# Kernel optimization log

Measured on AMD Instinct MI355X. Metric: run time of the kernel, lower is better.

The kernel has to match this reference:

```python
import jax, jax.numpy as jnp
import numpy as np

HIDDEN = 3584
N_HEADS = 28
N_KV = 4
HEAD_DIM = 128
MROPE = [16, 24, 24]          # sums to HEAD_DIM // 2
W_BITS = 4                    # per-output-channel symmetric weight fake-quant
A_BITS = 8                    # per-tensor symmetric activation fake-quant
ROPE_THETA = 1000000.0
B, S = 1, 2048


def fake_quant(x, bits, axis=None):
    """Symmetric uniform fake-quant with straight-through estimator."""
    qmax = 2.0 ** (bits - 1) - 1
    if axis is None:
        s = jnp.max(jnp.abs(x)) / qmax
    else:
        s = jnp.max(jnp.abs(x), axis=axis, keepdims=True) / qmax
    s = jnp.maximum(s, 1e-8)
    dq = jnp.clip(jnp.round(x / s), -qmax - 1.0, qmax) * s
    return x + jax.lax.stop_gradient(dq - x)


def quant_linear(x, w, b):
    """QuantLinear: fake-quant activations (per-tensor) and weights (per out-channel)."""
    xq = fake_quant(x, A_BITS)
    wq = fake_quant(w, W_BITS, axis=1)        # w: [out, in]
    y = xq @ wq.T
    return y + b if b is not None else y


def rotate_half(x):
    x1, x2 = jnp.split(x, 2, axis=-1)
    return jnp.concatenate([-x2, x1], axis=-1)


def apply_multimodal_rope(q, k, cos, sin):
    """cos/sin: (3, b, s, head_dim). Interleave t/h/w sections per mrope_section."""
    splits = np.cumsum([m * 2 for m in MROPE])[:-1]

    def mix(t):
        parts = jnp.split(t, splits, axis=-1)
        return jnp.concatenate([parts[i][i % 3] for i in range(len(parts))], axis=-1)[:, None]  # (b,1,s,hd)

    c, s_ = mix(cos), mix(sin)
    q_emb = q * c + rotate_half(q) * s_
    k_emb = k * c + rotate_half(k) * s_
    return q_emb, k_emb


def setup_inputs() -> dict:
    key = jax.random.key(0)
    ks = jax.random.split(key, 8)
    hidden_states = jax.random.normal(ks[0], (B, S, HIDDEN), dtype=jnp.float32)
    # realistic rotary embeddings, broadcast over the 3 mrope axes (text: all equal)
    inv_freq = 1.0 / (ROPE_THETA ** (np.arange(0, HEAD_DIM, 2, dtype=np.float32) / HEAD_DIM))
    pos = np.arange(S, dtype=np.float32)
    freqs = pos[:, None] * inv_freq[None, :]                  # (S, hd/2)
    emb = np.concatenate([freqs, freqs], axis=-1)             # (S, hd)
    cos = jnp.asarray(np.broadcast_to(np.cos(emb)[None, None], (3, B, S, HEAD_DIM)).copy())
    sin = jnp.asarray(np.broadcast_to(np.sin(emb)[None, None], (3, B, S, HEAD_DIM)).copy())
    sc = 0.02
    wq = jax.random.normal(ks[1], (HIDDEN, HIDDEN), dtype=jnp.float32) * sc
    bq = jax.random.normal(ks[2], (HIDDEN,), dtype=jnp.float32) * sc
    wk = jax.random.normal(ks[3], (N_KV * HEAD_DIM, HIDDEN), dtype=jnp.float32) * sc
    bk = jax.random.normal(ks[4], (N_KV * HEAD_DIM,), dtype=jnp.float32) * sc
    wv = jax.random.normal(ks[5], (N_KV * HEAD_DIM, HIDDEN), dtype=jnp.float32) * sc
    bv = jax.random.normal(ks[6], (N_KV * HEAD_DIM,), dtype=jnp.float32) * sc
    wo = jax.random.normal(ks[7], (HIDDEN, HIDDEN), dtype=jnp.float32) * sc
    return {"hidden_states": hidden_states, "cos": cos, "sin": sin,
            "wq": wq, "bq": bq, "wk": wk, "bk": bk, "wv": wv, "bv": bv, "wo": wo}


def reference(hidden_states, cos, sin, wq, bq, wk, bk, wv, bv, wo):
    b, s, _ = hidden_states.shape
    q = quant_linear(hidden_states, wq, bq).reshape(b, s, N_HEADS, HEAD_DIM).transpose(0, 2, 1, 3)
    k = quant_linear(hidden_states, wk, bk).reshape(b, s, N_KV, HEAD_DIM).transpose(0, 2, 1, 3)
    v = quant_linear(hidden_states, wv, bv).reshape(b, s, N_KV, HEAD_DIM).transpose(0, 2, 1, 3)
    q, k = apply_multimodal_rope(q, k, cos, sin)
    g = N_HEADS // N_KV
    k = jnp.repeat(k, g, axis=1)   # repeat_kv
    v = jnp.repeat(v, g, axis=1)
    scores = jnp.einsum('bhqd,bhkd->bhqk', q, k) / np.float32(np.sqrt(HEAD_DIM))
    causal = jnp.tril(jnp.ones((s, s), dtype=bool))
    scores = jnp.where(causal[None, None], scores, jnp.finfo(scores.dtype).min)
    p = jax.nn.softmax(scores, axis=-1)
    attn = jnp.einsum('bhqk,bhkd->bhqd', p, v)
    attn = attn.transpose(0, 2, 1, 3).reshape(b, s, N_HEADS * HEAD_DIM)
    return quant_linear(attn, wo, None)
```

## Files before the change

### kernel.cpp

```cpp
#include <hip/hip_runtime.h>
#include <stdint.h>


#define S_LEN 2048
#define HID   3584
#define NH    28
#define NKV   4
#define HD    128
#define GQA   7
#define KD    3584

typedef signed char i8;
typedef unsigned short u16;
typedef __attribute__((ext_vector_type(4))) int      v4i;
typedef __attribute__((ext_vector_type(4))) float    v4f;
typedef __attribute__((ext_vector_type(8))) _Float16 f16x8;
typedef __attribute__((ext_vector_type(4))) float    f32x4;

#define QK_SCALE   4096.0f
#define S_UNSCALE  5.9604644775390625e-8f
#define V_SCALE    64.0f
#define P_SCALE    16384.0f
#define O_UNSCALE  9.5367431640625e-7f

#define GLOAD_LDS(g, l) __builtin_amdgcn_global_load_lds( \
    (__attribute__((address_space(1))) void*)(g),          \
    (__attribute__((address_space(3))) void*)(l), 16, 0, 0)

static __device__ __forceinline__ u16 f16bits(_Float16 h) {
  u16 u; __builtin_memcpy(&u, &h, 2); return u;
}
static __device__ __forceinline__ void splitf16(float x, u16& hb, u16& lb) {
  _Float16 h = (_Float16)x;
  float r = x - (float)h;
  _Float16 l = (_Float16)r;
  hb = f16bits(h); lb = f16bits(l);
}

__global__ void k_zero(float* p) {
  if (threadIdx.x < 8) p[threadIdx.x] = 0.0f;
}

__global__ void k_absmax(const float* __restrict__ x, long long n, unsigned* __restrict__ out) {
  long long i0 = ((long long)blockIdx.x * blockDim.x + threadIdx.x) * 4;
  long long stride = (long long)gridDim.x * blockDim.x * 4;
  float m = 0.0f;
  for (long long i = i0; i < n; i += stride) {
    f32x4 v = *(const f32x4*)(x + i);
    m = fmaxf(m, fmaxf(fmaxf(fabsf(v.x), fabsf(v.y)), fmaxf(fabsf(v.z), fabsf(v.w))));
  }
  #pragma unroll
  for (int o = 32; o > 0; o >>= 1) m = fmaxf(m, __shfl_xor(m, o, 64));
  __shared__ float sm[4];
  if ((threadIdx.x & 63) == 0) sm[threadIdx.x >> 6] = m;
  __syncthreads();
  if (threadIdx.x == 0) {
    m = fmaxf(fmaxf(sm[0], sm[1]), fmaxf(sm[2], sm[3]));
    atomicMax(out, __float_as_uint(m));
  }
}

__global__ void k_quant_act(const float* __restrict__ x, i8* __restrict__ q,
                            const unsigned* __restrict__ amax, long long n) {
  float s = fmaxf(__uint_as_float(*amax) / 127.0f, 1e-8f);
  long long i = ((long long)blockIdx.x * blockDim.x + threadIdx.x) * 4;
  if (i >= n) return;
  f32x4 v = *(const f32x4*)(x + i);
  char4 c;
  c.x = (char)fminf(fmaxf(rintf(v.x / s), -128.0f), 127.0f);
  c.y = (char)fminf(fmaxf(rintf(v.y / s), -128.0f), 127.0f);
  c.z = (char)fminf(fmaxf(rintf(v.z / s), -128.0f), 127.0f);
  c.w = (char)fminf(fmaxf(rintf(v.w / s), -128.0f), 127.0f);
  *(char4*)(q + i) = c;
}

__global__ void k_quant_w(const float* __restrict__ w, i8* __restrict__ wq,
                          float* __restrict__ sw) {
  const int row = blockIdx.x;
  const float2* wr = (const float2*)(w + (long long)row * KD);
  float2 v[7];
  float m = 0.0f;
  #pragma unroll
  for (int j = 0; j < 7; j++) {
    v[j] = wr[threadIdx.x + 256 * j];
    m = fmaxf(m, fmaxf(fabsf(v[j].x), fabsf(v[j].y)));
  }
  #pragma unroll
  for (int o = 32; o > 0; o >>= 1) m = fmaxf(m, __shfl_xor(m, o, 64));
  __shared__ float sm[4];
  if ((threadIdx.x & 63) == 0) sm[threadIdx.x >> 6] = m;
  __syncthreads();
  const float mm = fmaxf(fmaxf(sm[0], sm[1]), fmaxf(sm[2], sm[3]));
  const float s = fmaxf(mm / 7.0f, 1e-8f);
  if (threadIdx.x == 0) sw[row] = s;
  u16* o = (u16*)(wq + (long long)row * KD);
  #pragma unroll
  for (int j = 0; j < 7; j++) {
    const int c0 = (int)fminf(fmaxf(rintf(v[j].x / s), -8.0f), 7.0f);
    const int c1 = (int)fminf(fmaxf(rintf(v[j].y / s), -8.0f), 7.0f);
    o[threadIdx.x + 256 * j] = (u16)((c0 & 0xff) | ((c1 & 0xff) << 8));
  }
}

__global__ __launch_bounds__(256, 3) void k_gemm(
    const i8* __restrict__ Aq,
    const i8* __restrict__ W0, const i8* __restrict__ W1, const i8* __restrict__ W2,
    const float* __restrict__ sw0, const float* __restrict__ sw1, const float* __restrict__ sw2,
    const float* __restrict__ b0, const float* __restrict__ b1, const float* __restrict__ b2,
    const float* __restrict__ cosb, const float* __restrict__ sinb,
    const unsigned* __restrict__ amax_slot,
    u16* __restrict__ qhi, u16* __restrict__ qlo,
    u16* __restrict__ khi, u16* __restrict__ klo,
    u16* __restrict__ vthi, u16* __restrict__ vtlo,
    float* __restrict__ outO, int kind) {
  __shared__ i8 As[128 * 64];
  __shared__ i8 Bs[128 * 64];
  const int tid = threadIdx.x, wid = tid >> 6, lane = tid & 63;

  const int q8 = (int)gridDim.x >> 3;
  const int orig = blockIdx.x;
  const int wgid = (orig & 7) * q8 + (orig >> 3);
  const int ct = wgid >> 4;
  const int mb = wgid & 15;

  const i8* Bw; const float* sw; const float* bias; int epi; int nbase;
  if (kind == 1)      { Bw = W0; sw = sw0; bias = nullptr; epi = 3; nbase = ct * 128; }
  else if (ct < 28)   { Bw = W0; sw = sw0; bias = b0;      epi = 0; nbase = ct * 128; }
  else if (ct < 32)   { Bw = W1; sw = sw1; bias = b1;      epi = 1; nbase = (ct - 28) * 128; }
  else                { Bw = W2; sw = sw2; bias = b2;      epi = 2; nbase = (ct - 32) * 128; }

  const float s_a = fmaxf(__uint_as_float(*amax_slot) / 127.0f, 1e-8f);

  v4i acc[2][8];
  #pragma unroll
  for (int a = 0; a < 2; a++)
    #pragma unroll
    for (int b = 0; b < 8; b++) acc[a][b] = (v4i)(0);

  const long long arow0 = (long long)mb * 128 * KD;
  const long long brow0 = (long long)nbase * KD;

  for (int kt = 0; kt < KD / 64; ++kt) {
    const int k0 = kt * 64;
    #pragma unroll
    for (int j = 0; j < 2; j++) {
      const int c = tid + 256 * j;
      const int r = c >> 2, seg = c & 3;
      const int so = (seg ^ ((r >> 1) & 3)) << 4;
      GLOAD_LDS(Aq + arow0 + (long long)r * KD + k0 + so, As + c * 16);
      GLOAD_LDS(Bw + brow0 + (long long)r * KD + k0 + so, Bs + c * 16);
    }
    __syncthreads();
    v4i af[2];
    #pragma unroll
    for (int mt = 0; mt < 2; mt++) {
      const int rl = wid * 32 + mt * 16 + (lane & 15);
      af[mt] = *(const v4i*)(As + rl * 64 + ((((lane >> 4)) ^ ((rl >> 1) & 3)) << 4));
    }
    #pragma unroll
    for (int nt = 0; nt < 8; nt++) {
      const int rb = nt * 16 + (lane & 15);
      const v4i bfr = *(const v4i*)(Bs + rb * 64 + ((((lane >> 4)) ^ ((rb >> 1) & 3)) << 4));
      acc[0][nt] = __builtin_amdgcn_mfma_i32_16x16x64_i8(af[0], bfr, acc[0][nt], 0, 0, 0);
      acc[1][nt] = __builtin_amdgcn_mfma_i32_16x16x64_i8(af[1], bfr, acc[1][nt], 0, 0, 0);
    }
    __syncthreads();
  }

  float y[2][8][4];
  #pragma unroll
  for (int mt = 0; mt < 2; mt++)
    #pragma unroll
    for (int nt = 0; nt < 8; nt++) {
      const int n = nbase + nt * 16 + (lane & 15);
      const float sc = s_a * sw[n];
      const float bb = bias ? bias[n] : 0.0f;
      #pragma unroll
      for (int r = 0; r < 4; r++) y[mt][nt][r] = sc * (float)acc[mt][nt][r] + bb;
    }

  if (epi == 3) {
    #pragma unroll
    for (int mt = 0; mt < 2; mt++)
      #pragma unroll
      for (int r = 0; r < 4; r++) {
        const int m_ = mb * 128 + wid * 32 + mt * 16 + ((lane >> 4) << 2) + r;
        #pragma unroll
        for (int nt = 0; nt < 8; nt++)
          outO[(long long)m_ * HID + ct * 128 + nt * 16 + (lane & 15)] = y[mt][nt][r];
      }
  } else if (epi == 2) {
    const int gkv = ct - 32;
    #pragma unroll
    for (int mt = 0; mt < 2; mt++)
      #pragma unroll
      for (int nt = 0; nt < 8; nt++) {
        const int d = nt * 16 + (lane & 15);
        const int mbase = mb * 128 + wid * 32 + mt * 16 + ((lane >> 4) << 2);
        ushort4 hv, lv;
        #pragma unroll
        for (int r = 0; r < 4; r++)
          splitf16(y[mt][nt][r] * V_SCALE, ((u16*)&hv)[r], ((u16*)&lv)[r]);
        const long long o = ((long long)(gkv * HD + d)) * S_LEN + mbase;
        *(ushort4*)(vthi + o) = hv;
        *(ushort4*)(vtlo + o) = lv;
      }
  } else {
    const int head = (epi == 0) ? ct : (ct - 28);
    u16* oh = (epi == 0) ? qhi : khi;
    u16* ol = (epi == 0) ? qlo : klo;
    const float qs = (epi == 0) ? 0.08838834764831845f * QK_SCALE : QK_SCALE;
    #pragma unroll
    for (int mt = 0; mt < 2; mt++)
      #pragma unroll
      for (int r = 0; r < 4; r++) {
        const int m_ = mb * 128 + wid * 32 + mt * 16 + ((lane >> 4) << 2) + r;
        #pragma unroll
        for (int nt = 0; nt < 8; nt++) {
          const int d = nt * 16 + (lane & 15);
          const int sec = (d < 32) ? 0 : ((d < 80) ? 1 : 2);
          const long long ci = ((long long)sec * S_LEN + m_) * HD + d;
          const float c = cosb[ci], s = sinb[ci];
          const float part = (nt < 4) ? -y[mt][nt + 4][r] : y[mt][nt - 4][r];
          const float e = (y[mt][nt][r] * c + part * s) * qs;
          const long long o = ((long long)head * S_LEN + m_) * HD + d;
          splitf16(e, oh[o], ol[o]);
        }
      }
  }
}

__global__ __launch_bounds__(256, 1) void k_attn(
    const u16* __restrict__ qhi, const u16* __restrict__ qlo,
    const u16* __restrict__ khi, const u16* __restrict__ klo,
    const u16* __restrict__ vthi, const u16* __restrict__ vtlo,
    float* __restrict__ attn, unsigned* __restrict__ amax) {
  const int orig = blockIdx.x;
  const int nchunk = (int)gridDim.x >> 3;
  const int swz = (orig & 7) * nchunk + (orig >> 3);
  const int h = swz >> 3;
  const int p = swz & 7;
  const int g = h / GQA;
  const int tid = threadIdx.x, wid = tid >> 6, lane = tid & 63;

  __shared__ u16 KH[2][64 * 128], KL[2][64 * 128];
  __shared__ u16 VH[2][128 * 64], VL[2][128 * 64];

#define STAGE(b, t) do {                                                        \
    const int s0_ = (t) * 64;                                                   \
    _Pragma("unroll")                                                           \
    for (int j_ = 0; j_ < 4; j_++) {                                            \
      const int c_ = tid + 256 * j_;                                            \
      const int r_ = c_ >> 4, sg_ = c_ & 15;                                    \
      const long long gb_ = ((long long)g * S_LEN + s0_ + r_) * HD +            \
                            ((sg_ ^ (r_ & 7)) << 3);                            \
      GLOAD_LDS(khi + gb_, (i8*)KH[(b)] + c_ * 16);                             \
      GLOAD_LDS(klo + gb_, (i8*)KL[(b)] + c_ * 16);                             \
    }                                                                           \
    _Pragma("unroll")                                                           \
    for (int j_ = 0; j_ < 4; j_++) {                                            \
      const int c_ = tid + 256 * j_;                                            \
      const int d_ = c_ >> 3, sg_ = c_ & 7;                                     \
      const long long gb_ = ((long long)(g * HD + d_)) * S_LEN + s0_ +          \
                            ((sg_ ^ (d_ & 7)) << 3);                            \
      GLOAD_LDS(vthi + gb_, (i8*)VH[(b)] + c_ * 16);                            \
      GLOAD_LDS(vtlo + gb_, (i8*)VL[(b)] + c_ * 16);                            \
    }                                                                           \
  } while (0)

  float am = 0.0f;

  for (int pass = 0; pass < 2; ++pass) {
    const int qt = pass ? p : 15 - p;
    const int ktn = 2 * qt + 2;

    STAGE(0, 0);

    f16x8 qh[2][4], ql[2][4];
    #pragma unroll
    for (int mt = 0; mt < 2; mt++) {
      const int row = qt * 128 + wid * 32 + mt * 16 + (lane & 15);
      const long long base = ((long long)h * S_LEN + row) * HD + ((lane >> 4) << 3);
      #pragma unroll
      for (int kc = 0; kc < 4; kc++) {
        qh[mt][kc] = *(const f16x8*)(qhi + base + kc * 32);
        ql[mt][kc] = *(const f16x8*)(qlo + base + kc * 32);
      }
    }

    v4f O[2][8];
    #pragma unroll
    for (int a = 0; a < 2; a++)
      #pragma unroll
      for (int b = 0; b < 8; b++) O[a][b] = (v4f)(0.0f);
    float mrun[2][4], lsum[2][4];
    #pragma unroll
    for (int a = 0; a < 2; a++)
      #pragma unroll
      for (int r = 0; r < 4; r++) { mrun[a][r] = -1e30f; lsum[a][r] = 0.0f; }

    const int qmaxw = qt * 128 + wid * 32 + 31;
    __syncthreads();

    for (int s = 0; s < ktn; ++s) {
      const int cur = s & 1;
      const int s0 = s * 64;
      u16* PH = KH[cur] + wid * 2048;
      u16* PL = KL[cur] + wid * 2048;

      if (s + 1 < ktn) STAGE(cur ^ 1, s + 1);

      const bool active = (s0 <= qmaxw);
      v4f S[2][4];
      if (active) {
        #pragma unroll
        for (int a = 0; a < 2; a++)
          #pragma unroll
          for (int b = 0; b < 4; b++) S[a][b] = (v4f)(0.0f);
        __builtin_amdgcn_s_setprio(1);
        #pragma unroll
        for (int kc = 0; kc < 4; kc++) {
          #pragma unroll
          for (int nt = 0; nt < 4; nt++) {
            const int rk = nt * 16 + (lane & 15);
            const int ch = kc * 4 + (lane >> 4);
            const int idx = rk * 128 + ((ch ^ (rk & 7)) << 3);
            const f16x8 kh = *(const f16x8*)(KH[cur] + idx);
            const f16x8 kl = *(const f16x8*)(KL[cur] + idx);
            #pragma unroll
            for (int mt = 0; mt < 2; mt++) {
              S[mt][nt] = __builtin_amdgcn_mfma_f32_16x16x32_f16(qh[mt][kc], kh, S[mt][nt], 0, 0, 0);
              S[mt][nt] = __builtin_amdgcn_mfma_f32_16x16x32_f16(qh[mt][kc], kl, S[mt][nt], 0, 0, 0);
              S[mt][nt] = __builtin_amdgcn_mfma_f32_16x16x32_f16(ql[mt][kc], kh, S[mt][nt], 0, 0, 0);
            }
          }
        }
        __builtin_amdgcn_s_setprio(0);
        #pragma unroll
        for (int mt = 0; mt < 2; mt++)
          #pragma unroll
          for (int r = 0; r < 4; r++) {
            const int q_g = qt * 128 + wid * 32 + mt * 16 + ((lane >> 4) << 2) + r;
            float sv[4];
            float tm = -1e30f;
            #pragma unroll
            for (int nt = 0; nt < 4; nt++) {
              const int kp = s0 + nt * 16 + (lane & 15);
              sv[nt] = (kp <= q_g) ? S[mt][nt][r] * S_UNSCALE : -1e30f;
              tm = fmaxf(tm, sv[nt]);
            }
            tm = fmaxf(tm, __shfl_xor(tm, 1, 64));
            tm = fmaxf(tm, __shfl_xor(tm, 2, 64));
            tm = fmaxf(tm, __shfl_xor(tm, 4, 64));
            tm = fmaxf(tm, __shfl_xor(tm, 8, 64));
            const float nm = fmaxf(mrun[mt][r], tm);
            const float rs = __expf(mrun[mt][r] - nm);
            mrun[mt][r] = nm;
            float ps = 0.0f;
            #pragma unroll
            for (int nt = 0; nt < 4; nt++) {
              const float pv = (sv[nt] > -1e29f) ? __expf(sv[nt] - nm) : 0.0f;
              ps += pv;
              S[mt][nt][r] = pv;
            }
            ps += __shfl_xor(ps, 1, 64);
            ps += __shfl_xor(ps, 2, 64);
            ps += __shfl_xor(ps, 4, 64);
            ps += __shfl_xor(ps, 8, 64);
            if (rs != 1.0f) {
              lsum[mt][r] = lsum[mt][r] * rs + ps;
              #pragma unroll
              for (int nt = 0; nt < 8; nt++) O[mt][nt][r] *= rs;
            } else {
              lsum[mt][r] += ps;
            }
          }
      }
      __syncthreads();

      if (active) {
        #pragma unroll
        for (int mt = 0; mt < 2; mt++)
          #pragma unroll
          for (int r = 0; r < 4; r++) {
            const int q_l = mt * 16 + ((lane >> 4) << 2) + r;
            #pragma unroll
            for (int nt = 0; nt < 4; nt++) {
              const int kp_l = nt * 16 + (lane & 15);
              const int ch = kp_l >> 3;
              const int idx = q_l * 64 + ((ch ^ (q_l & 7)) << 3) + (kp_l & 7);
              splitf16(S[mt][nt][r] * P_SCALE, PH[idx], PL[idx]);
            }
          }
        #pragma unroll
        for (int kc = 0; kc < 2; kc++) {
          f16x8 pa[2], pb[2];
          #pragma unroll
          for (int mt = 0; mt < 2; mt++) {
            const int rq = mt * 16 + (lane & 15);
            const int ch = kc * 4 + (lane >> 4);
            const int idx = rq * 64 + ((ch ^ (rq & 7)) << 3);
            pa[mt] = *(const f16x8*)&PH[idx];
            pb[mt] = *(const f16x8*)&PL[idx];
          }
          __builtin_amdgcn_s_setprio(1);
          #pragma unroll
          for (int nt = 0; nt < 8; nt++) {
            const int rd = nt * 16 + (lane & 15);
            const int ch = kc * 4 + (lane >> 4);
            const int idx = rd * 64 + ((ch ^ (rd & 7)) << 3);
            const f16x8 vh = *(const f16x8*)(VH[cur] + idx);
            const f16x8 vl = *(const f16x8*)(VL[cur] + idx);
            #pragma unroll
            for (int mt = 0; mt < 2; mt++) {
              O[mt][nt] = __builtin_amdgcn_mfma_f32_16x16x32_f16(pa[mt], vh, O[mt][nt], 0, 0, 0);
              O[mt][nt] = __builtin_amdgcn_mfma_f32_16x16x32_f16(pb[mt], vh, O[mt][nt], 0, 0, 0);
              O[mt][nt] = __builtin_amdgcn_mfma_f32_16x16x32_f16(pa[mt], vl, O[mt][nt], 0, 0, 0);
            }
          }
          __builtin_amdgcn_s_setprio(0);
        }
      }
      __syncthreads();
    }

    #pragma unroll
    for (int mt = 0; mt < 2; mt++)
      #pragma unroll
      for (int r = 0; r < 4; r++) {
        const int q_g = qt * 128 + wid * 32 + mt * 16 + ((lane >> 4) << 2) + r;
        const float inv = O_UNSCALE / lsum[mt][r];
        #pragma unroll
        for (int nt = 0; nt < 8; nt++) {
          const float val = O[mt][nt][r] * inv;
          attn[(long long)q_g * HID + h * HD + nt * 16 + (lane & 15)] = val;
          am = fmaxf(am, fabsf(val));
        }
      }
  }
#undef STAGE

  am = fmaxf(am, __shfl_xor(am, 1, 64));
  am = fmaxf(am, __shfl_xor(am, 2, 64));
  am = fmaxf(am, __shfl_xor(am, 4, 64));
  am = fmaxf(am, __shfl_xor(am, 8, 64));
  am = fmaxf(am, __shfl_xor(am, 16, 64));
  am = fmaxf(am, __shfl_xor(am, 32, 64));
  if (lane == 0) atomicMax(amax, __float_as_uint(am));
}

extern "C" void kernel_launch(void* const* d_in, const int* in_sizes, int n_in,
                              void* d_out, int out_size, void* d_ws, size_t ws_size,
                              hipStream_t stream) {
  const float* hidden = (const float*)d_in[0];
  const float* cosb   = (const float*)d_in[1];
  const float* sinb   = (const float*)d_in[2];
  const float* wq     = (const float*)d_in[3];
  const float* bq     = (const float*)d_in[4];
  const float* wk     = (const float*)d_in[5];
  const float* bk     = (const float*)d_in[6];
  const float* wv     = (const float*)d_in[7];
  const float* bv     = (const float*)d_in[8];
  const float* wo     = (const float*)d_in[9];
  float* out = (float*)d_out;

  char* w = (char*)d_ws;
  size_t off = 0;
  auto alloc = [&](size_t bytes) -> void* {
    void* p = w + off;
    off += (bytes + 255) & ~(size_t)255;
    return p;
  };
  unsigned* scal = (unsigned*)alloc(256);
  i8* xq8   = (i8*)alloc((size_t)S_LEN * KD);
  i8* wq8   = (i8*)alloc((size_t)HID * KD);
  i8* wk8   = (i8*)alloc((size_t)NKV * HD * KD);
  i8* wv8   = (i8*)alloc((size_t)NKV * HD * KD);
  i8* wo8   = (i8*)alloc((size_t)HID * KD);
  float* swq = (float*)alloc(HID * 4);
  float* swk = (float*)alloc(NKV * HD * 4);
  float* swv = (float*)alloc(NKV * HD * 4);
  float* swo = (float*)alloc(HID * 4);
  u16* qhi_  = (u16*)alloc((size_t)NH * S_LEN * HD * 2);
  u16* qlo_  = (u16*)alloc((size_t)NH * S_LEN * HD * 2);
  u16* khi_  = (u16*)alloc((size_t)NKV * S_LEN * HD * 2);
  u16* klo_  = (u16*)alloc((size_t)NKV * S_LEN * HD * 2);
  u16* vthi_ = (u16*)alloc((size_t)NKV * S_LEN * HD * 2);
  u16* vtlo_ = (u16*)alloc((size_t)NKV * S_LEN * HD * 2);
  float* attnb = (float*)alloc((size_t)S_LEN * HID * 4);

  const long long nact = (long long)S_LEN * KD;

  k_zero<<<1, 64, 0, stream>>>((float*)scal);
  k_absmax<<<1024, 256, 0, stream>>>(hidden, nact, scal + 0);
  k_quant_w<<<HID, 256, 0, stream>>>(wq, wq8, swq);
  k_quant_w<<<NKV * HD, 256, 0, stream>>>(wk, wk8, swk);
  k_quant_w<<<NKV * HD, 256, 0, stream>>>(wv, wv8, swv);
  k_quant_w<<<HID, 256, 0, stream>>>(wo, wo8, swo);
  k_quant_act<<<(int)(nact / 4 / 256), 256, 0, stream>>>(hidden, xq8, scal + 0, nact);

  k_gemm<<<dim3(36 * 16), 256, 0, stream>>>(
      xq8, wq8, wk8, wv8, swq, swk, swv, bq, bk, bv, cosb, sinb, scal + 0,
      qhi_, qlo_, khi_, klo_, vthi_, vtlo_, nullptr, 0);

  k_attn<<<dim3(NH * 8), 256, 0, stream>>>(qhi_, qlo_, khi_, klo_, vthi_, vtlo_,
                                           attnb, scal + 1);

  k_quant_act<<<(int)(nact / 4 / 256), 256, 0, stream>>>(attnb, xq8, scal + 1, nact);

  k_gemm<<<dim3(28 * 16), 256, 0, stream>>>(
      xq8, wo8, nullptr, nullptr, swo, nullptr, nullptr, nullptr, nullptr, nullptr,
      nullptr, nullptr, scal + 1,
      nullptr, nullptr, nullptr, nullptr, nullptr, nullptr, out, 1);
}
```

Measured before the change: 558.1 us.

## Split attention query tile across eight waves of sixteen rows each

The attention kernel moves from 4 waves each owning 32 query rows to 8 waves each owning 16 rows, with 512 threads per block. K/V staging is spread over twice as many threads, and per-wave register state (Q fragments, O accumulators, softmax stats) is halved. The aim is more waves to hide latency and a lower per-wave register count. The cost is that each K/V fragment read from LDS now feeds half as many MFMAs, so LDS traffic per unit of compute doubles. Causal skipping also becomes finer-grained per wave.

```diff
diff --git a/kernel.cpp b/kernel.cpp
--- a/kernel.cpp
+++ b/kernel.cpp
@@ -230,7 +230,7 @@
   }
 }
 
-__global__ __launch_bounds__(256, 1) void k_attn(
+__global__ __launch_bounds__(512, 2) void k_attn(
     const u16* __restrict__ qhi, const u16* __restrict__ qlo,
     const u16* __restrict__ khi, const u16* __restrict__ klo,
     const u16* __restrict__ vthi, const u16* __restrict__ vtlo,
@@ -249,8 +249,8 @@
 #define STAGE(b, t) do {                                                        \
     const int s0_ = (t) * 64;                                                   \
     _Pragma("unroll")                                                           \
-    for (int j_ = 0; j_ < 4; j_++) {                                            \
-      const int c_ = tid + 256 * j_;                                            \
+    for (int j_ = 0; j_ < 2; j_++) {                                            \
+      const int c_ = tid + 512 * j_;                                            \
       const int r_ = c_ >> 4, sg_ = c_ & 15;                                    \
       const long long gb_ = ((long long)g * S_LEN + s0_ + r_) * HD +            \
                             ((sg_ ^ (r_ & 7)) << 3);                            \
@@ -258,8 +258,8 @@
       GLOAD_LDS(klo + gb_, (i8*)KL[(b)] + c_ * 16);                             \
     }                                                                           \
     _Pragma("unroll")                                                           \
-    for (int j_ = 0; j_ < 4; j_++) {                                            \
-      const int c_ = tid + 256 * j_;                                            \
+    for (int j_ = 0; j_ < 2; j_++) {                                            \
+      const int c_ = tid + 512 * j_;                                            \
       const int d_ = c_ >> 3, sg_ = c_ & 7;                                     \
       const long long gb_ = ((long long)(g * HD + d_)) * S_LEN + s0_ +          \
                             ((sg_ ^ (d_ & 7)) << 3);                            \
@@ -276,47 +276,40 @@
 
     STAGE(0, 0);
 
-    f16x8 qh[2][4], ql[2][4];
-    #pragma unroll
-    for (int mt = 0; mt < 2; mt++) {
-      const int row = qt * 128 + wid * 32 + mt * 16 + (lane & 15);
+    f16x8 qh[4], ql[4];
+    {
+      const int row = qt * 128 + wid * 16 + (lane & 15);
       const long long base = ((long long)h * S_LEN + row) * HD + ((lane >> 4) << 3);
       #pragma unroll
       for (int kc = 0; kc < 4; kc++) {
-        qh[mt][kc] = *(const f16x8*)(qhi + base + kc * 32);
-        ql[mt][kc] = *(const f16x8*)(qlo + base + kc * 32);
-      }
-    }
-
-    v4f O[2][8];
-    #pragma unroll
-    for (int a = 0; a < 2; a++)
-      #pragma unroll
-      for (int b = 0; b < 8; b++) O[a][b] = (v4f)(0.0f);
-    float mrun[2][4], lsum[2][4];
-    #pragma unroll
-    for (int a = 0; a < 2; a++)
-      #pragma unroll
-      for (int r = 0; r < 4; r++) { mrun[a][r] = -1e30f; lsum[a][r] = 0.0f; }
-
-    const int qmaxw = qt * 128 + wid * 32 + 31;
+        qh[kc] = *(const f16x8*)(qhi + base + kc * 32);
+        ql[kc] = *(const f16x8*)(qlo + base + kc * 32);
+      }
+    }
+
+    v4f O[8];
+    #pragma unroll
+    for (int b = 0; b < 8; b++) O[b] = (v4f)(0.0f);
+    float mrun[4], lsum[4];
+    #pragma unroll
+    for (int r = 0; r < 4; r++) { mrun[r] = -1e30f; lsum[r] = 0.0f; }
+
+    const int qmaxw = qt * 128 + wid * 16 + 15;
     __syncthreads();
 
     for (int s = 0; s < ktn; ++s) {
       const int cur = s & 1;
       const int s0 = s * 64;
-      u16* PH = KH[cur] + wid * 2048;
-      u16* PL = KL[cur] + wid * 2048;
+      u16* PH = KH[cur] + wid * 1024;
+      u16* PL = KL[cur] + wid * 1024;
 
       if (s + 1 < ktn) STAGE(cur ^ 1, s + 1);
 
       const bool active = (s0 <= qmaxw);
-      v4f S[2][4];
+      v4f S[4];
       if (active) {
         #pragma unroll
-        for (int a = 0; a < 2; a++)
-          #pragma unroll
-          for (int b = 0; b < 4; b++) S[a][b] = (v4f)(0.0f);
+        for (int b = 0; b < 4; b++) S[b] = (v4f)(0.0f);
         __builtin_amdgcn_s_setprio(1);
         #pragma unroll
         for (int kc = 0; kc < 4; kc++) {
@@ -327,81 +320,73 @@
             const int idx = rk * 128 + ((ch ^ (rk & 7)) << 3);
             const f16x8 kh = *(const f16x8*)(KH[cur] + idx);
             const f16x8 kl = *(const f16x8*)(KL[cur] + idx);
-            #pragma unroll
-            for (int mt = 0; mt < 2; mt++) {
-              S[mt][nt] = __builtin_amdgcn_mfma_f32_16x16x32_f16(qh[mt][kc], kh, S[mt][nt], 0, 0, 0);
-              S[mt][nt] = __builtin_amdgcn_mfma_f32_16x16x32_f16(qh[mt][kc], kl, S[mt][nt], 0, 0, 0);
-              S[mt][nt] = __builtin_amdgcn_mfma_f32_16x16x32_f16(ql[mt][kc], kh, S[mt][nt], 0, 0, 0);
-            }
+            S[nt] = __builtin_amdgcn_mfma_f32_16x16x32_f16(qh[kc], kh, S[nt], 0, 0, 0);
+            S[nt] = __builtin_amdgcn_mfma_f32_16x16x32_f16(qh[kc], kl, S[nt], 0, 0, 0);
+            S[nt] = __builtin_amdgcn_mfma_f32_16x16x32_f16(ql[kc], kh, S[nt], 0, 0, 0);
           }
         }
         __builtin_amdgcn_s_setprio(0);
         #pragma unroll
-        for (int mt = 0; mt < 2; mt++)
+        for (int r = 0; r < 4; r++) {
+          const int q_g = qt * 128 + wid * 16 + ((lane >> 4) << 2) + r;
+          float sv[4];
+          float tm = -1e30f;
           #pragma unroll
-          for (int r = 0; r < 4; r++) {
-            const int q_g = qt * 128 + wid * 32 + mt * 16 + ((lane >> 4) << 2) + r;
-            float sv[4];
-            float tm = -1e30f;
+          for (int nt = 0; nt < 4; nt++) {
+            const int kp = s0 + nt * 16 + (lane & 15);
+            sv[nt] = (kp <= q_g) ? S[nt][r] * S_UNSCALE : -1e30f;
+            tm = fmaxf(tm, sv[nt]);
+          }
+          tm = fmaxf(tm, __shfl_xor(tm, 1, 64));
+          tm = fmaxf(tm, __shfl_xor(tm, 2, 64));
+          tm = fmaxf(tm, __shfl_xor(tm, 4, 64));
+          tm = fmaxf(tm, __shfl_xor(tm, 8, 64));
+          const float nm = fmaxf(mrun[r], tm);
+          const float rs = __expf(mrun[r] - nm);
+          mrun[r] = nm;
+          float ps = 0.0f;
+          #pragma unroll
+          for (int nt = 0; nt < 4; nt++) {
+            const float pv = (sv[nt] > -1e29f) ? __expf(sv[nt] - nm) : 0.0f;
+            ps += pv;
+            S[nt][r] = pv;
+          }
+          ps += __shfl_xor(ps, 1, 64);
+          ps += __shfl_xor(ps, 2, 64);
+          ps += __shfl_xor(ps, 4, 64);
+          ps += __shfl_xor(ps, 8, 64);
+          if (rs != 1.0f) {
+            lsum[r] = lsum[r] * rs + ps;
             #pragma unroll
-            for (int nt = 0; nt < 4; nt++) {
-              const int kp = s0 + nt * 16 + (lane & 15);
-              sv[nt] = (kp <= q_g) ? S[mt][nt][r] * S_UNSCALE : -1e30f;
-              tm = fmaxf(tm, sv[nt]);
-            }
-            tm = fmaxf(tm, __shfl_xor(tm, 1, 64));
-            tm = fmaxf(tm, __shfl_xor(tm, 2, 64));
-            tm = fmaxf(tm, __shfl_xor(tm, 4, 64));
-            tm = fmaxf(tm, __shfl_xor(tm, 8, 64));
-            const float nm = fmaxf(mrun[mt][r], tm);
-            const float rs = __expf(mrun[mt][r] - nm);
-            mrun[mt][r] = nm;
-            float ps = 0.0f;
-            #pragma unroll
-            for (int nt = 0; nt < 4; nt++) {
-              const float pv = (sv[nt] > -1e29f) ? __expf(sv[nt] - nm) : 0.0f;
-              ps += pv;
-              S[mt][nt][r] = pv;
-            }
-            ps += __shfl_xor(ps, 1, 64);
-            ps += __shfl_xor(ps, 2, 64);
-            ps += __shfl_xor(ps, 4, 64);
-            ps += __shfl_xor(ps, 8, 64);
-            if (rs != 1.0f) {
-              lsum[mt][r] = lsum[mt][r] * rs + ps;
-              #pragma unroll
-              for (int nt = 0; nt < 8; nt++) O[mt][nt][r] *= rs;
-            } else {
-              lsum[mt][r] += ps;
-            }
-          }
+            for (int nt = 0; nt < 8; nt++) O[nt][r] *= rs;
+          } else {
+            lsum[r] += ps;
+          }
+        }
       }
       __syncthreads();
 
       if (active) {
         #pragma unroll
-        for (int mt = 0; mt < 2; mt++)
+        for (int r = 0; r < 4; r++) {
+          const int q_l = ((lane >> 4) << 2) + r;
           #pragma unroll
-          for (int r = 0; r < 4; r++) {
-            const int q_l = mt * 16 + ((lane >> 4) << 2) + r;
-            #pragma unroll
-            for (int nt = 0; nt < 4; nt++) {
-              const int kp_l = nt * 16 + (lane & 15);
-              const int ch = kp_l >> 3;
-              const int idx = q_l * 64 + ((ch ^ (q_l & 7)) << 3) + (kp_l & 7);
-              splitf16(S[mt][nt][r] * P_SCALE, PH[idx], PL[idx]);
-            }
-          }
+          for (int nt = 0; nt < 4; nt++) {
+            const int kp_l = nt * 16 + (lane & 15);
+            const int ch = kp_l >> 3;
+            const int idx = q_l * 64 + ((ch ^ (q_l & 7)) << 3) + (kp_l & 7);
+            splitf16(S[nt][r] * P_SCALE, PH[idx], PL[idx]);
+          }
+        }
         #pragma unroll
         for (int kc = 0; kc < 2; kc++) {
-          f16x8 pa[2], pb[2];
-          #pragma unroll
-          for (int mt = 0; mt < 2; mt++) {
-            const int rq = mt * 16 + (lane & 15);
+          f16x8 pa, pb;
+          {
+            const int rq = lane & 15;
             const int ch = kc * 4 + (lane >> 4);
             const int idx = rq * 64 + ((ch ^ (rq & 7)) << 3);
-            pa[mt] = *(const f16x8*)&PH[idx];
-            pb[mt] = *(const f16x8*)&PL[idx];
+            pa = *(const f16x8*)&PH[idx];
+            pb = *(const f16x8*)&PL[idx];
           }
           __builtin_amdgcn_s_setprio(1);
           #pragma unroll
@@ -411,12 +396,9 @@
             const int idx = rd * 64 + ((ch ^ (rd & 7)) << 3);
             const f16x8 vh = *(const f16x8*)(VH[cur] + idx);
             const f16x8 vl = *(const f16x8*)(VL[cur] + idx);
-            #pragma unroll
-            for (int mt = 0; mt < 2; mt++) {
-              O[mt][nt] = __builtin_amdgcn_mfma_f32_16x16x32_f16(pa[mt], vh, O[mt][nt], 0, 0, 0);
-              O[mt][nt] = __builtin_amdgcn_mfma_f32_16x16x32_f16(pb[mt], vh, O[mt][nt], 0, 0, 0);
-              O[mt][nt] = __builtin_amdgcn_mfma_f32_16x16x32_f16(pa[mt], vl, O[mt][nt], 0, 0, 0);
-            }
+            O[nt] = __builtin_amdgcn_mfma_f32_16x16x32_f16(pa, vh, O[nt], 0, 0, 0);
+            O[nt] = __builtin_amdgcn_mfma_f32_16x16x32_f16(pb, vh, O[nt], 0, 0, 0);
+            O[nt] = __builtin_amdgcn_mfma_f32_16x16x32_f16(pa, vl, O[nt], 0, 0, 0);
           }
           __builtin_amdgcn_s_setprio(0);
         }
@@ -425,18 +407,16 @@
     }
 
     #pragma unroll
-    for (int mt = 0; mt < 2; mt++)
-      #pragma unroll
-      for (int r = 0; r < 4; r++) {
-        const int q_g = qt * 128 + wid * 32 + mt * 16 + ((lane >> 4) << 2) + r;
-        const float inv = O_UNSCALE / lsum[mt][r];
-        #pragma unroll
-        for (int nt = 0; nt < 8; nt++) {
-          const float val = O[mt][nt][r] * inv;
-          attn[(long long)q_g * HID + h * HD + nt * 16 + (lane & 15)] = val;
-          am = fmaxf(am, fabsf(val));
-        }
-      }
+    for (int r = 0; r < 4; r++) {
+      const int q_g = qt * 128 + wid * 16 + ((lane >> 4) << 2) + r;
+      const float inv = O_UNSCALE / lsum[r];
+      #pragma unroll
+      for (int nt = 0; nt < 8; nt++) {
+        const float val = O[nt][r] * inv;
+        attn[(long long)q_g * HID + h * HD + nt * 16 + (lane & 15)] = val;
+        am = fmaxf(am, fabsf(val));
+      }
+    }
   }
 #undef STAGE
 
@@ -503,7 +483,7 @@
       xq8, wq8, wk8, wv8, swq, swk, swv, bq, bk, bv, cosb, sinb, scal + 0,
       qhi_, qlo_, khi_, klo_, vthi_, vtlo_, nullptr, 0);
 
-  k_attn<<<dim3(NH * 8), 256, 0, stream>>>(qhi_, qlo_, khi_, klo_, vthi_, vtlo_,
+  k_attn<<<dim3(NH * 8), 512, 0, stream>>>(qhi_, qlo_, khi_, klo_, vthi_, vtlo_,
                                            attnb, scal + 1);
 
   k_quant_act<<<(int)(nact / 4 / 256), 256, 0, stream>>>(attnb, xq8, scal + 1, nact);
```

Measured after the change: 600.0 us. 1.07x slower.
